# Kernel optimization log

Hardware: AMD Instinct MI355X
Metric: run time of the kernel (lower is better)

Reference implementation:

```python
import jax, jax.numpy as jnp
import numpy as np

N_HEAD, D_MODEL, D_HEAD = 16, 1024, 64
BSZ, SEQ = 4, 2048
SCALE = 1.0 / D_HEAD ** 0.5
LN_EPS = 1e-5
NEG = -1e10


def layer_norm(x, gamma, beta):
    mu = jnp.mean(x, axis=-1, keepdims=True)
    var = jnp.var(x, axis=-1, keepdims=True)
    return (x - mu) * jax.lax.rsqrt(var + LN_EPS) * gamma + beta


def setup_inputs() -> dict:
    key = jax.random.key(0)
    ks = jax.random.split(key, 8)
    q = jax.random.normal(ks[0], (BSZ, SEQ, D_MODEL), dtype=jnp.float32)
    attn_mask = jax.random.randint(ks[1], (SEQ, SEQ), 0, 2).astype(bool)
    s = 1.0 / np.sqrt(D_MODEL)
    Wq = jax.random.normal(ks[2], (D_MODEL, N_HEAD * D_HEAD), dtype=jnp.float32) * s
    Wk = jax.random.normal(ks[3], (D_MODEL, N_HEAD * D_HEAD), dtype=jnp.float32) * s
    Wv = jax.random.normal(ks[4], (D_MODEL, N_HEAD * D_HEAD), dtype=jnp.float32) * s
    Wo = jax.random.normal(ks[5], (N_HEAD * D_HEAD, D_MODEL), dtype=jnp.float32) * s
    gamma = jnp.ones((D_MODEL,), dtype=jnp.float32)
    beta = jnp.zeros((D_MODEL,), dtype=jnp.float32)
    return {"q": q, "attn_mask": attn_mask, "Wq": Wq, "Wk": Wk, "Wv": Wv,
            "Wo": Wo, "gamma": gamma, "beta": beta}


def reference(q, attn_mask, Wq, Wk, Wv, Wo, gamma, beta):
    # pre_lnorm: residual uses the normalized q (as in the torch code, q is reassigned)
    qn = layer_norm(q, gamma, beta)                      # (b, n1, d_model)
    hq = (qn @ Wq).reshape(BSZ, SEQ, N_HEAD, D_HEAD)     # self-attn: k = v = q
    hk = (qn @ Wk).reshape(BSZ, SEQ, N_HEAD, D_HEAD)
    hv = (qn @ Wv).reshape(BSZ, SEQ, N_HEAD, D_HEAD)
    score = jnp.einsum('bind,bjnd->ijbn', hq, hk) * SCALE  # (n1, n2, b, h)
    score = jnp.where(attn_mask[:, :, None, None], NEG, score)
    prob = jax.nn.softmax(score, axis=1)
    vec = jnp.einsum('ijbn,bjnd->bind', prob, hv).reshape(BSZ, SEQ, N_HEAD * D_HEAD)
    attn_out = vec @ Wo
    return qn + attn_out
```

## Files before the change

kernel.cpp:

```cpp
#include <hip/hip_runtime.h>

typedef __bf16 bf16;
typedef __bf16 bf16x8 __attribute__((ext_vector_type(8)));
typedef __bf16 bf16x4 __attribute__((ext_vector_type(4)));
typedef float  f32x4  __attribute__((ext_vector_type(4)));

#define MFMA16 __builtin_amdgcn_mfma_f32_16x16x32_bf16

static constexpr int   BSZ   = 4;
static constexpr int   SEQL  = 2048;
static constexpr int   DM    = 1024;
static constexpr int   NHEAD = 16;
static constexpr int   DHEAD = 64;
static constexpr float SCL2  = 0.125f * 1.44269504f;

__device__ __forceinline__ void glds16(bf16* lds, const bf16* g) {
    __builtin_amdgcn_global_load_lds(
        (const __attribute__((address_space(1))) unsigned int*)g,
        (__attribute__((address_space(3))) unsigned int*)lds, 16, 0, 0);
}

__global__ void detect_mask(const unsigned int* __restrict__ m, int* __restrict__ flag) {
    __shared__ int ok[4];
    if (threadIdx.x < 4) ok[threadIdx.x] = 1;
    __syncthreads();
    for (int i = 0; i < 16; ++i) {
        unsigned int w = m[threadIdx.x * 16 + i];
        if (!(w == 0u || w == 1u)) ok[0] = 0;
        if (w & 0xFEFEFEFEu) ok[1] = 0;
        if (!(w == 0u || w == 0x3F800000u)) ok[2] = 0;
        unsigned lo = w & 0xFFFFu, hi = w >> 16;
        if (!((lo == 0u || lo == 0x3F80u) && (hi == 0u || hi == 0x3F80u))) ok[3] = 0;
    }
    __syncthreads();
    if (threadIdx.x == 0)
        *flag = ok[0] ? 0 : (ok[1] ? 1 : (ok[2] ? 2 : 3));
}

__device__ __forceinline__ bool mask_at(const void* m, int fl, long idx) {
    if (fl == 0) return ((const int*)m)[idx] != 0;
    if (fl == 1) return ((const unsigned char*)m)[idx] != 0;
    if (fl == 2) return ((const float*)m)[idx] != 0.0f;
    return ((const unsigned short*)m)[idx] != 0;
}

__global__ __launch_bounds__(256) void prep_bits(const void* __restrict__ mask,
                                                 const int* __restrict__ flagp,
                                                 unsigned long long* __restrict__ rb) {
    const int fl = *flagp;
    const int word = blockIdx.x * 4 + (threadIdx.x >> 6);
    const long base = (long)word * 64 + (threadIdx.x & 63);
    unsigned long long b = __ballot(mask_at(mask, fl, base));
    if ((threadIdx.x & 63) == 0) rb[word] = b;
}

__global__ __launch_bounds__(256) void prep_words(
    const unsigned long long* __restrict__ rb, unsigned long long* __restrict__ wm)
{
    const int t = threadIdx.x, L = t & 63, w = t >> 6;
    const int pair = blockIdx.x * 4 + w;
    const int qgrp = pair >> 5, kt = pair & 31;
    const unsigned long long r0 = rb[(size_t)(qgrp * 16 + (L & 15)) * 32 + kt];
    const int lq = L >> 4;
    unsigned long long myw = 0;
    #pragma unroll
    for (int jr = 0; jr < 16; ++jr) {
        const int jj = jr >> 2, r = jr & 3;
        const int bitpos = (jj & 1) * 32 + lq * 8 + (jj >> 1) * 4 + r;
        unsigned long long bal = __ballot(((r0 >> bitpos) & 1ull) != 0ull);
        if (L == jr) myw = bal;
    }
    if (L < 16) wm[(size_t)pair * 16 + L] = myw;
}

__global__ __launch_bounds__(256) void ln_kernel(
    const float* __restrict__ x, const float* __restrict__ g,
    const float* __restrict__ bta, bf16* __restrict__ y)
{
    const int row = blockIdx.x, t = threadIdx.x;
    const float4 v = ((const float4*)(x + (size_t)row * DM))[t];
    float s  = v.x + v.y + v.z + v.w;
    float ss = v.x * v.x + v.y * v.y + v.z * v.z + v.w * v.w;
    for (int m = 32; m >= 1; m >>= 1) { s += __shfl_xor(s, m); ss += __shfl_xor(ss, m); }
    __shared__ float red[8];
    const int w = t >> 6, L = t & 63;
    if (L == 0) { red[w] = s; red[4 + w] = ss; }
    __syncthreads();
    s  = red[0] + red[1] + red[2] + red[3];
    ss = red[4] + red[5] + red[6] + red[7];
    const float mu = s * (1.0f / DM);
    const float var = ss * (1.0f / DM) - mu * mu;
    const float r = rsqrtf(var + 1e-5f);
    const float4 gv = ((const float4*)g)[t];
    const float4 bv = ((const float4*)bta)[t];
    bf16x4 o;
    o[0] = (bf16)((v.x - mu) * r * gv.x + bv.x);
    o[1] = (bf16)((v.y - mu) * r * gv.y + bv.y);
    o[2] = (bf16)((v.z - mu) * r * gv.z + bv.z);
    o[3] = (bf16)((v.w - mu) * r * gv.w + bv.w);
    ((bf16x4*)(y + (size_t)row * DM))[t] = o;
}

__global__ void cvt_w(const float* __restrict__ Wq, const float* __restrict__ Wk,
                      const float* __restrict__ Wv, const float* __restrict__ Wo,
                      bf16* __restrict__ Wt)
{
    __shared__ float tile[32][33];
    const int z = blockIdx.z;
    const float* src = (z == 0) ? Wq : (z == 1) ? Wk : (z == 2) ? Wv : Wo;
    const float scl = (z == 1) ? SCL2 : 1.0f;
    bf16* dst = Wt + (size_t)z * DM * DM;
    const int tx = threadIdx.x, ty = threadIdx.y;
    const int nIn = blockIdx.x * 32 + tx;
    const int kIn = blockIdx.y * 32;
    for (int i = 0; i < 32; i += 8)
        tile[ty + i][tx] = src[(size_t)(kIn + ty + i) * DM + nIn];
    __syncthreads();
    const int nOut = blockIdx.x * 32;
    const int kOut = blockIdx.y * 32 + tx;
    for (int i = 0; i < 32; i += 8)
        dst[(size_t)(nOut + ty + i) * DM + kOut] = (bf16)(tile[tx][ty + i] * scl);
}

__device__ __forceinline__ void gemm128_core(
    const bf16* __restrict__ A, const bf16* __restrict__ Bt,
    int m0, int n0, bool swapped, f32x4 acc[4][4], bf16* Asm, bf16* Bsm)
{
    const int t = threadIdx.x, w = t >> 6, L = t & 63;
    const int lr = L & 15, lq = L >> 4;
    const int wm = w & 1, wn = w >> 1;
    const int srow = L >> 3;
    const int scol = ((L & 7) ^ (L >> 3)) * 8;
    const bf16* Ab = A  + (size_t)(m0 + w * 32 + srow) * DM + scol;
    const bf16* Bb = Bt + (size_t)(n0 + w * 32 + srow) * DM + scol;
    bf16* AsmW = Asm + (w * 32) * 64;
    bf16* BsmW = Bsm + (w * 32) * 64;
    for (int kk = 0; kk < DM; kk += 64) {
        __syncthreads();
        glds16(AsmW,           Ab + kk);
        glds16(AsmW +  8 * 64, Ab + (size_t) 8 * DM + kk);
        glds16(AsmW + 16 * 64, Ab + (size_t)16 * DM + kk);
        glds16(AsmW + 24 * 64, Ab + (size_t)24 * DM + kk);
        glds16(BsmW,           Bb + kk);
        glds16(BsmW +  8 * 64, Bb + (size_t) 8 * DM + kk);
        glds16(BsmW + 16 * 64, Bb + (size_t)16 * DM + kk);
        glds16(BsmW + 24 * 64, Bb + (size_t)24 * DM + kk);
        __syncthreads();
        #pragma unroll
        for (int ks = 0; ks < 2; ++ks) {
            bf16x8 af[4], bf_[4];
            #pragma unroll
            for (int i = 0; i < 4; ++i) {
                const int ra = wm * 64 + i * 16 + lr;
                af[i] = *(const bf16x8*)(Asm + ra * 64 + ((((ks << 2) | lq) ^ (lr & 7)) << 3));
            }
            #pragma unroll
            for (int j = 0; j < 4; ++j) {
                const int rb2 = wn * 64 + j * 16 + lr;
                bf_[j] = *(const bf16x8*)(Bsm + rb2 * 64 + ((((ks << 2) | lq) ^ (lr & 7)) << 3));
            }
            if (!swapped) {
                #pragma unroll
                for (int i = 0; i < 4; ++i)
                    #pragma unroll
                    for (int j = 0; j < 4; ++j)
                        acc[i][j] = MFMA16(af[i], bf_[j], acc[i][j], 0, 0, 0);
            } else {
                #pragma unroll
                for (int i = 0; i < 4; ++i)
                    #pragma unroll
                    for (int j = 0; j < 4; ++j)
                        acc[i][j] = MFMA16(bf_[j], af[i], acc[i][j], 0, 0, 0);
            }
        }
    }
}

__global__ __launch_bounds__(256) void qkv128(
    const bf16* __restrict__ qn, const bf16* __restrict__ Wt,
    bf16* __restrict__ Qb, bf16* __restrict__ Kb, bf16* __restrict__ Vtb)
{
    __shared__ __align__(16) bf16 Asm[128 * 64];
    __shared__ __align__(16) bf16 Bsm[128 * 64];
    const int ny = blockIdx.y;
    const int z = ny >> 3;
    const int m0 = blockIdx.x * 128, n0 = (ny & 7) * 128;
    f32x4 acc[4][4] = {};
    gemm128_core(qn, Wt + (size_t)z * DM * DM, m0, n0, z < 2, acc, Asm, Bsm);
    const int t = threadIdx.x, L = t & 63, w = t >> 6;
    const int wm = w & 1, wn = w >> 1, lr = L & 15, lq = L >> 4;
    if (z < 2) {
        bf16* dst = z ? Kb : Qb;
        #pragma unroll
        for (int i = 0; i < 4; ++i) {
            const int m = m0 + wm * 64 + i * 16 + lr;
            const int b = m >> 11, s = m & 2047;
            #pragma unroll
            for (int j = 0; j < 4; ++j) {
                const int n = n0 + wn * 64 + j * 16 + lq * 4;
                const int h = n >> 6, d = n & 63;
                bf16x4 ov;
                #pragma unroll
                for (int r = 0; r < 4; ++r) ov[r] = (bf16)acc[i][j][r];
                *(bf16x4*)(dst + (((size_t)b * NHEAD + h) * SEQL + s) * DHEAD + d) = ov;
            }
        }
    } else {
        #pragma unroll
        for (int j = 0; j < 4; ++j) {
            const int n = n0 + wn * 64 + j * 16 + lr;
            const int h = n >> 6, d = n & 63;
            #pragma unroll
            for (int i = 0; i < 4; ++i) {
                const int m = m0 + wm * 64 + i * 16 + lq * 4;
                const int b = m >> 11, s = m & 2047;
                bf16x4 ov;
                #pragma unroll
                for (int r = 0; r < 4; ++r) ov[r] = (bf16)acc[i][j][r];
                *(bf16x4*)(Vtb + (((size_t)b * NHEAD + h) * DHEAD + d) * SEQL + s) = ov;
            }
        }
    }
}

__global__ __launch_bounds__(256) void out128(
    const bf16* __restrict__ vec, const bf16* __restrict__ Wot,
    const bf16* __restrict__ qnb, float* __restrict__ out)
{
    __shared__ __align__(16) bf16 Asm[128 * 64];
    __shared__ __align__(16) bf16 Bsm[128 * 64];
    const int m0 = blockIdx.x * 128, n0 = blockIdx.y * 128;
    f32x4 acc[4][4] = {};
    gemm128_core(vec, Wot, m0, n0, true, acc, Asm, Bsm);
    const int t = threadIdx.x, L = t & 63, w = t >> 6;
    const int wm = w & 1, wn = w >> 1, lr = L & 15, lq = L >> 4;
    #pragma unroll
    for (int i = 0; i < 4; ++i) {
        const int m = m0 + wm * 64 + i * 16 + lr;
        #pragma unroll
        for (int j = 0; j < 4; ++j) {
            const int n = n0 + wn * 64 + j * 16 + lq * 4;
            const size_t idx = (size_t)m * DM + n;
            const bf16x4 q4 = *(const bf16x4*)(qnb + idx);
            float4 ov;
            ov.x = acc[i][j][0] + (float)q4[0];
            ov.y = acc[i][j][1] + (float)q4[1];
            ov.z = acc[i][j][2] + (float)q4[2];
            ov.w = acc[i][j][3] + (float)q4[3];
            *(float4*)(out + idx) = ov;
        }
    }
}

__global__ __launch_bounds__(512) void flash_attn(
    const bf16* __restrict__ Qb, const bf16* __restrict__ Kb,
    const bf16* __restrict__ Vtb, const unsigned long long* __restrict__ mb,
    bf16* __restrict__ vec)
{
    __shared__ __align__(16) bf16 Ksm [2][64 * 72];
    __shared__ __align__(16) bf16 Vtsm[2][64 * 72];

    const int t = threadIdx.x, w = t >> 6, L = t & 63;
    const int lr = L & 15, lq = L >> 4;
    const int bid = blockIdx.x;
    const int slot = bid & 7, rest = bid >> 3;
    const int qblk = rest & 7;
    const int bh = ((rest >> 3) << 3) + slot;
    const int b = bh >> 4, h = bh & 15;
    const int q0 = qblk * 256 + w * 32;

    const bf16* Qh  = Qb  + (size_t)bh * SEQL * DHEAD;
    const bf16* Kh  = Kb  + (size_t)bh * SEQL * DHEAD;
    const bf16* Vth = Vtb + (size_t)bh * DHEAD * SEQL;

    bf16x8 qf[2][2];
    #pragma unroll
    for (int qg = 0; qg < 2; ++qg)
        #pragma unroll
        for (int ks = 0; ks < 2; ++ks)
            qf[qg][ks] = *(const bf16x8*)(Qh + (size_t)(q0 + qg * 16 + lr) * DHEAD + ks * 32 + lq * 8);

    const int qgrp0 = __builtin_amdgcn_readfirstlane(q0 >> 4);
    const unsigned long long* wm0 = mb + (size_t)qgrp0 * 512;
    const unsigned long long* wm1 = wm0 + 512;

    f32x4 o[4][2] = {};
    f32x4 lacc[2] = {};

    const bf16 one = (bf16)1.0f;
    const bf16x8 ones8 = {one, one, one, one, one, one, one, one};
    const float fz = 0.0f;

    const int sr = t >> 3, sc = (t & 7) * 8;
    const int zrow = ((sr >> 2) & 1) * 32 + ((sr >> 5) & 1) * 16 + ((sr >> 3) & 3) * 4 + (sr & 3);
    constexpr int NT = SEQL / 64;
    bf16x8 kreg, vreg;

    kreg = *(const bf16x8*)(Kh  + (size_t)sr * DHEAD + sc);
    vreg = *(const bf16x8*)(Vth + (size_t)sr * SEQL + sc);
    *(bf16x8*)(Ksm[0]  + zrow * 72 + sc) = kreg;
    *(bf16x8*)(Vtsm[0] + sr * 72 + sc)   = vreg;
    kreg = *(const bf16x8*)(Kh  + (size_t)(64 + sr) * DHEAD + sc);
    vreg = *(const bf16x8*)(Vth + (size_t)sr * SEQL + 64 + sc);
    __syncthreads();

    for (int kt = 0; kt < NT; ++kt) {
        const int cur = kt & 1;
        const bf16* Kc = Ksm[cur];
        const bf16* Vc = Vtsm[cur];

        f32x4 s[4][2] = {};
        #pragma unroll
        for (int ks = 0; ks < 2; ++ks) {
            bf16x8 kf[4];
            #pragma unroll
            for (int jj = 0; jj < 4; ++jj)
                kf[jj] = *(const bf16x8*)(Kc + (jj * 16 + lr) * 72 + ks * 32 + lq * 8);
            __builtin_amdgcn_s_setprio(1);
            #pragma unroll
            for (int jj = 0; jj < 4; ++jj)
                #pragma unroll
                for (int qg = 0; qg < 2; ++qg)
                    s[jj][qg] = MFMA16(kf[jj], qf[qg][ks], s[jj][qg], 0, 0, 0);
            __builtin_amdgcn_s_setprio(0);
        }

        if (kt + 1 < NT) {
            *(bf16x8*)(Ksm [cur ^ 1] + zrow * 72 + sc) = kreg;
            *(bf16x8*)(Vtsm[cur ^ 1] + sr * 72 + sc)   = vreg;
            if (kt + 2 < NT) {
                const int kb2 = (kt + 2) * 64;
                kreg = *(const bf16x8*)(Kh  + (size_t)(kb2 + sr) * DHEAD + sc);
                vreg = *(const bf16x8*)(Vth + (size_t)sr * SEQL + kb2 + sc);
            }
        }

        bf16x8 pf[2][2];
        #pragma unroll
        for (int qg = 0; qg < 2; ++qg) {
            const unsigned long long* wp = (qg ? wm1 : wm0) + kt * 16;
            #pragma unroll
            for (int ks = 0; ks < 2; ++ks) {
                bf16x8 pv;
                #pragma unroll
                for (int r = 0; r < 4; ++r) {
                    float e0 = __builtin_amdgcn_exp2f(s[ks][qg][r]);
                    float e1 = __builtin_amdgcn_exp2f(s[2 + ks][qg][r]);
                    float z0, z1;
                    asm("v_cndmask_b32 %0, %1, %2, %3"
                        : "=v"(z0) : "v"(e0), "v"(fz), "s"(wp[ks * 4 + r]));
                    asm("v_cndmask_b32 %0, %1, %2, %3"
                        : "=v"(z1) : "v"(e1), "v"(fz), "s"(wp[(2 + ks) * 4 + r]));
                    pv[r]     = (bf16)z0;
                    pv[4 + r] = (bf16)z1;
                }
                pf[qg][ks] = pv;
            }
        }

        __builtin_amdgcn_s_setprio(1);
        #pragma unroll
        for (int ks = 0; ks < 2; ++ks) {
            #pragma unroll
            for (int qg = 0; qg < 2; ++qg)
                lacc[qg] = MFMA16(ones8, pf[qg][ks], lacc[qg], 0, 0, 0);
            #pragma unroll
            for (int dg = 0; dg < 4; ++dg) {
                bf16x8 vf = *(const bf16x8*)(Vc + (dg * 16 + lr) * 72 + ks * 32 + lq * 8);
                #pragma unroll
                for (int qg = 0; qg < 2; ++qg)
                    o[dg][qg] = MFMA16(vf, pf[qg][ks], o[dg][qg], 0, 0, 0);
            }
        }
        __builtin_amdgcn_s_setprio(0);

        if (kt + 1 < NT) {
            asm volatile("s_waitcnt lgkmcnt(0)" ::: "memory");
            __builtin_amdgcn_s_barrier();
        }
    }

    #pragma unroll
    for (int qg = 0; qg < 2; ++qg) {
        const float rl = 1.0f / lacc[qg][0];
        const size_t rowb = ((size_t)b * SEQL + q0 + qg * 16 + lr) * DM + h * DHEAD;
        #pragma unroll
        for (int dg = 0; dg < 4; ++dg) {
            bf16x4 ov;
            #pragma unroll
            for (int r = 0; r < 4; ++r) ov[r] = (bf16)(o[dg][qg][r] * rl);
            *(bf16x4*)(vec + rowb + dg * 16 + lq * 4) = ov;
        }
    }
}

extern "C" void kernel_launch(void* const* d_in, const int* in_sizes, int n_in,
                              void* d_out, int out_size, void* d_ws, size_t ws_size,
                              hipStream_t stream)
{
    const float* qin   = (const float*)d_in[0];
    const void*  mask  = d_in[1];
    const float* Wq    = (const float*)d_in[2];
    const float* Wk    = (const float*)d_in[3];
    const float* Wv    = (const float*)d_in[4];
    const float* Wo    = (const float*)d_in[5];
    const float* gamma = (const float*)d_in[6];
    const float* beta  = (const float*)d_in[7];
    float* out = (float*)d_out;

    char* w = (char*)d_ws;
    int*  flag = (int*)w;
    bf16* qnb  = (bf16*)(w + 256);
    bf16* Wt   = qnb + (size_t)8192 * 1024;
    bf16* Qb   = Wt + (size_t)4 * 1024 * 1024;
    bf16* Kb   = Qb + (size_t)8192 * 1024;
    bf16* Vtb  = Kb + (size_t)8192 * 1024;
    bf16* vec  = Vtb + (size_t)8192 * 1024;
    unsigned long long* rbits  = (unsigned long long*)(vec + (size_t)8192 * 1024);
    unsigned long long* mwords = rbits + 65536;

    detect_mask<<<1, 256, 0, stream>>>((const unsigned int*)mask, flag);
    prep_bits<<<SEQL * (SEQL / 64) / 4, 256, 0, stream>>>(mask, flag, rbits);
    prep_words<<<1024, 256, 0, stream>>>(rbits, mwords);
    ln_kernel<<<8192, 256, 0, stream>>>(qin, gamma, beta, qnb);
    cvt_w<<<dim3(32, 32, 4), dim3(32, 8), 0, stream>>>(Wq, Wk, Wv, Wo, Wt);
    qkv128<<<dim3(64, 24), 256, 0, stream>>>(qnb, Wt, Qb, Kb, Vtb);
    flash_attn<<<512, 512, 0, stream>>>(Qb, Kb, Vtb, mwords, vec);
    out128<<<dim3(64, 8), 256, 0, stream>>>(vec, Wt + (size_t)3 * 1024 * 1024, qnb, out);
}
```

Before: 293.5 us.

## Double-buffer GEMM LDS tiles with K-step 32 and prefetch next tile

Restructures the shared GEMM core used by the QKV and output projections. It now uses two 128x32 LDS buffers per operand and issues the global-to-LDS loads for the next K slice before running the MFMAs on the current one, aiming to overlap memory latency with compute. The K step is halved to 32 and the XOR swizzle on the LDS layout is dropped. The unswizzled 64-byte row stride may bring LDS bank conflicts on the fragment reads, and the smaller K step means more loop iterations and barriers per FLOP.

Result: slower. 314.8 us (+7.3%).

```diff
diff --git a/kernel.cpp b/kernel.cpp
--- a/kernel.cpp
+++ b/kernel.cpp
@@ -129,50 +129,53 @@
     const int t = threadIdx.x, w = t >> 6, L = t & 63;
     const int lr = L & 15, lq = L >> 4;
     const int wm = w & 1, wn = w >> 1;
-    const int srow = L >> 3;
-    const int scol = ((L & 7) ^ (L >> 3)) * 8;
+    const int srow = L >> 2, scol = (L & 3) * 8;
     const bf16* Ab = A  + (size_t)(m0 + w * 32 + srow) * DM + scol;
     const bf16* Bb = Bt + (size_t)(n0 + w * 32 + srow) * DM + scol;
-    bf16* AsmW = Asm + (w * 32) * 64;
-    bf16* BsmW = Bsm + (w * 32) * 64;
-    for (int kk = 0; kk < DM; kk += 64) {
-        __syncthreads();
-        glds16(AsmW,           Ab + kk);
-        glds16(AsmW +  8 * 64, Ab + (size_t) 8 * DM + kk);
-        glds16(AsmW + 16 * 64, Ab + (size_t)16 * DM + kk);
-        glds16(AsmW + 24 * 64, Ab + (size_t)24 * DM + kk);
-        glds16(BsmW,           Bb + kk);
-        glds16(BsmW +  8 * 64, Bb + (size_t) 8 * DM + kk);
-        glds16(BsmW + 16 * 64, Bb + (size_t)16 * DM + kk);
-        glds16(BsmW + 24 * 64, Bb + (size_t)24 * DM + kk);
-        __syncthreads();
-        #pragma unroll
-        for (int ks = 0; ks < 2; ++ks) {
-            bf16x8 af[4], bf_[4];
-            #pragma unroll
-            for (int i = 0; i < 4; ++i) {
-                const int ra = wm * 64 + i * 16 + lr;
-                af[i] = *(const bf16x8*)(Asm + ra * 64 + ((((ks << 2) | lq) ^ (lr & 7)) << 3));
-            }
-            #pragma unroll
-            for (int j = 0; j < 4; ++j) {
-                const int rb2 = wn * 64 + j * 16 + lr;
-                bf_[j] = *(const bf16x8*)(Bsm + rb2 * 64 + ((((ks << 2) | lq) ^ (lr & 7)) << 3));
-            }
-            if (!swapped) {
-                #pragma unroll
-                for (int i = 0; i < 4; ++i)
-                    #pragma unroll
-                    for (int j = 0; j < 4; ++j)
-                        acc[i][j] = MFMA16(af[i], bf_[j], acc[i][j], 0, 0, 0);
-            } else {
-                #pragma unroll
-                for (int i = 0; i < 4; ++i)
-                    #pragma unroll
-                    for (int j = 0; j < 4; ++j)
-                        acc[i][j] = MFMA16(bf_[j], af[i], acc[i][j], 0, 0, 0);
-            }
-        }
+    constexpr int BUF = 128 * 32;
+    bf16* AsmW = Asm + (w * 32) * 32;
+    bf16* BsmW = Bsm + (w * 32) * 32;
+
+    glds16(AsmW,           Ab);
+    glds16(AsmW + 16 * 32, Ab + (size_t)16 * DM);
+    glds16(BsmW,           Bb);
+    glds16(BsmW + 16 * 32, Bb + (size_t)16 * DM);
+    __syncthreads();
+
+    int cur = 0;
+    for (int kk = 0; kk < DM; kk += 32) {
+        if (kk + 32 < DM) {
+            bf16* Aa = AsmW + (cur ^ 1) * BUF;
+            bf16* Ba = BsmW + (cur ^ 1) * BUF;
+            glds16(Aa,           Ab + kk + 32);
+            glds16(Aa + 16 * 32, Ab + (size_t)16 * DM + kk + 32);
+            glds16(Ba,           Bb + kk + 32);
+            glds16(Ba + 16 * 32, Bb + (size_t)16 * DM + kk + 32);
+        }
+        const bf16* Ac = Asm + cur * BUF;
+        const bf16* Bc = Bsm + cur * BUF;
+        bf16x8 af[4], bf_[4];
+        #pragma unroll
+        for (int i = 0; i < 4; ++i)
+            af[i] = *(const bf16x8*)(Ac + (wm * 64 + i * 16 + lr) * 32 + lq * 8);
+        #pragma unroll
+        for (int j = 0; j < 4; ++j)
+            bf_[j] = *(const bf16x8*)(Bc + (wn * 64 + j * 16 + lr) * 32 + lq * 8);
+        if (!swapped) {
+            #pragma unroll
+            for (int i = 0; i < 4; ++i)
+                #pragma unroll
+                for (int j = 0; j < 4; ++j)
+                    acc[i][j] = MFMA16(af[i], bf_[j], acc[i][j], 0, 0, 0);
+        } else {
+            #pragma unroll
+            for (int i = 0; i < 4; ++i)
+                #pragma unroll
+                for (int j = 0; j < 4; ++j)
+                    acc[i][j] = MFMA16(bf_[j], af[i], acc[i][j], 0, 0, 0);
+        }
+        if (kk + 32 < DM) __syncthreads();
+        cur ^= 1;
     }
 }
 
@@ -180,8 +183,8 @@
     const bf16* __restrict__ qn, const bf16* __restrict__ Wt,
     bf16* __restrict__ Qb, bf16* __restrict__ Kb, bf16* __restrict__ Vtb)
 {
-    __shared__ __align__(16) bf16 Asm[128 * 64];
-    __shared__ __align__(16) bf16 Bsm[128 * 64];
+    __shared__ __align__(16) bf16 Asm[2 * 128 * 32];
+    __shared__ __align__(16) bf16 Bsm[2 * 128 * 32];
     const int ny = blockIdx.y;
     const int z = ny >> 3;
     const int m0 = blockIdx.x * 128, n0 = (ny & 7) * 128;
@@ -227,8 +230,8 @@
     const bf16* __restrict__ vec, const bf16* __restrict__ Wot,
     const bf16* __restrict__ qnb, float* __restrict__ out)
 {
-    __shared__ __align__(16) bf16 Asm[128 * 64];
-    __shared__ __align__(16) bf16 Bsm[128 * 64];
+    __shared__ __align__(16) bf16 Asm[2 * 128 * 32];
+    __shared__ __align__(16) bf16 Bsm[2 * 128 * 32];
     const int m0 = blockIdx.x * 128, n0 = blockIdx.y * 128;
     f32x4 acc[4][4] = {};
     gemm128_core(vec, Wot, m0, n0, true, acc, Asm, Bsm);
```
